# Kernel optimization log

Measured on AMD Instinct MI355X. Metric: run time of the kernel, lower is better.

## Reference

```python
import jax, jax.numpy as jnp
import numpy as np

EMBED_DIM = 1024
NUM_HEADS = 16
HEAD_DIM = EMBED_DIM // NUM_HEADS
SEQ_LEN = 2048
BATCH = 2
THETA_BASE = 10000.0


def rope_angles(head_dim, max_seq_len):
    inv_freq = 1.0 / (THETA_BASE ** (jnp.arange(0, head_dim, 2, dtype=jnp.float32) / head_dim))
    pos = jnp.arange(max_seq_len, dtype=jnp.float32)
    angles = pos[:, None] * inv_freq[None, :]              # [S, D/2]
    angles = jnp.concatenate([angles, angles], axis=-1)    # [S, D]
    return jnp.cos(angles), jnp.sin(angles)


def apply_rope(x, cos, sin):
    # x: [B, H, S, D]; cos/sin: [S, D]
    d = x.shape[-1]
    x1, x2 = x[..., : d // 2], x[..., d // 2 :]
    rotated = jnp.concatenate([-x2, x1], axis=-1)
    return x * cos[None, None, :, :] + rotated * sin[None, None, :, :]


def setup_inputs() -> dict:
    key = jax.random.key(0)
    kx, kq, kk, kv, ko = jax.random.split(key, 5)
    s = 1.0 / np.sqrt(EMBED_DIM)
    return {
        "x": jax.random.normal(kx, (BATCH, SEQ_LEN, EMBED_DIM), dtype=jnp.float32),
        "Wq": jax.random.normal(kq, (EMBED_DIM, EMBED_DIM), dtype=jnp.float32) * s,
        "Wk": jax.random.normal(kk, (EMBED_DIM, EMBED_DIM), dtype=jnp.float32) * s,
        "Wv": jax.random.normal(kv, (EMBED_DIM, EMBED_DIM), dtype=jnp.float32) * s,
        "Wo": jax.random.normal(ko, (EMBED_DIM, EMBED_DIM), dtype=jnp.float32) * s,
    }


def reference(x, Wq, Wk, Wv, Wo):
    B, S, E = x.shape
    H, D = NUM_HEADS, HEAD_DIM
    cos, sin = rope_angles(D, S)

    def split_heads(t):
        return t.reshape(B, S, H, D).transpose(0, 2, 1, 3)  # [B,H,S,D]

    q = split_heads(x @ Wq.T)
    k = split_heads(x @ Wk.T)
    v = split_heads(x @ Wv.T)

    q = apply_rope(q, cos, sin)
    k = apply_rope(k, cos, sin)

    scores = jnp.einsum("bhsd,bhtd->bhst", q, k)
    causal = jnp.triu(jnp.ones((S, S), dtype=bool), k=1)
    scores = jnp.where(causal[None, None, :, :], -jnp.inf, scores)
    weights = jax.nn.softmax(scores / jnp.sqrt(jnp.float32(D)), axis=-1)

    ctx = jnp.einsum("bhst,bhtd->bhsd", weights, v)
    ctx = ctx.transpose(0, 2, 1, 3).reshape(B, S, E)
    return ctx @ Wo.T
```

## Files before the change

kernel.cpp:

```cpp
#include <hip/hip_runtime.h>
#include <hip/hip_bf16.h>

#define H_NUM 16
#define D_DIM 64
#define S_LEN 2048
#define EMB   1024
#define M_TOT 4096

typedef unsigned short u16;
typedef unsigned int   u32;
typedef __attribute__((ext_vector_type(8))) short short8;
typedef __attribute__((ext_vector_type(4))) float f32x4;

__device__ __forceinline__ u32 f2bf_u(float f) {
    u32 u = __float_as_uint(f);
    return (u + 0x7fffu + ((u >> 16) & 1u)) >> 16;
}
__device__ __forceinline__ u32 pack2(float a, float b) {
    return f2bf_u(a) | (f2bf_u(b) << 16);
}
__device__ __forceinline__ u32 pack2t(float a, float b) {
    return __builtin_amdgcn_perm(__float_as_uint(b), __float_as_uint(a),
                                 0x07060302u);
}
__device__ __forceinline__ uint4 pack8(float4 lo, float4 hi) {
    return make_uint4(pack2(lo.x, lo.y), pack2(lo.z, lo.w),
                      pack2(hi.x, hi.y), pack2(hi.z, hi.w));
}

__device__ __forceinline__ void lds_dma16(const u16* g, u16* l) {
    __builtin_amdgcn_global_load_lds(
        (const __attribute__((address_space(1))) void*)g,
        (__attribute__((address_space(3))) void*)l, 16, 0, 0);
}

__global__ __launch_bounds__(256) void cast_kernel(
    const float* __restrict__ x,  const float* __restrict__ Wq,
    const float* __restrict__ Wk, const float* __restrict__ Wv,
    const float* __restrict__ Wo, u16* __restrict__ ws, float2* __restrict__ tab)
{
    const int seg = blockIdx.y;
    if (seg == 5) {
        const int idx = blockIdx.x * 256 + threadIdx.x;
        if (idx < S_LEN * 32) {
            const int s = idx >> 5, d = idx & 31;
            const float ang = (float)s * __expf(-(float)d * 0.28782313662425573f);
            tab[idx] = make_float2(cosf(ang), sinf(ang));
        }
        return;
    }
    const float* src = (seg == 0) ? x : (seg == 1) ? Wq : (seg == 2) ? Wk
                     : (seg == 3) ? Wv : Wo;
    u16* dst = (seg == 0) ? ws : ws + (3 + seg) * 1048576;
    const int n = (seg == 0) ? 4194304 : 1048576;
    const int idx = (blockIdx.x * 256 + threadIdx.x) * 8;
    if (idx < n) {
        float4 lo = *(const float4*)(src + idx);
        float4 hi = *(const float4*)(src + idx + 4);
        *(uint4*)(dst + idx) = pack8(lo, hi);
    }
}

__global__ __launch_bounds__(256) void qkv_rope_kernel(
    const u16* __restrict__ xb, const u16* __restrict__ wb,
    const float2* __restrict__ tab,
    u16* __restrict__ qo, u16* __restrict__ ko, u16* __restrict__ vo)
{
    const int w  = blockIdx.y >> 3;
    const int nb = blockIdx.y & 7;
    const u16* W = wb + w * 1048576;

    __shared__ __align__(16) u16 smem[12288];
    u16* As = smem;
    u16* Bs = smem + 64 * 64;
    u16 (*Ep)[132] = (u16(*)[132])smem;

    const int tid   = threadIdx.x;
    const int lane  = tid & 63;
    const int wid   = tid >> 6;
    const int waveM = wid >> 1;
    const int waveN = wid & 1;
    const int col16 = lane & 15;
    const int quad  = lane >> 4;

    const int m0 = blockIdx.x * 64;
    const int n0 = nb * 128;

    f32x4 acc[2][4];
    const f32x4 zero4 = {0.f, 0.f, 0.f, 0.f};
#pragma unroll
    for (int i = 0; i < 2; i++)
#pragma unroll
        for (int j = 0; j < 4; j++) acc[i][j] = zero4;

    const int drow = tid >> 3;
    const int dpos = tid & 7;
    const u16* Ag = xb + (size_t)m0 * EMB;
    const u16* Bg = W  + (size_t)n0 * EMB;

    for (int k0 = 0; k0 < EMB; k0 += 64) {
        __syncthreads();
#pragma unroll
        for (int j = 0; j < 2; j++) {
            const int rl = j * 32 + drow;
            const int cg = dpos ^ (rl & 7);
            lds_dma16(Ag + (size_t)rl * EMB + k0 + cg * 8,
                      As + (j * 32 + wid * 8) * 64);
        }
#pragma unroll
        for (int j = 0; j < 4; j++) {
            const int rl = j * 32 + drow;
            const int cg = dpos ^ (rl & 7);
            lds_dma16(Bg + (size_t)rl * EMB + k0 + cg * 8,
                      Bs + (j * 32 + wid * 8) * 64);
        }
        __syncthreads();

        short8 af[2][2], bf[4][2];
#pragma unroll
        for (int mt = 0; mt < 2; mt++) {
            const int r = waveM * 32 + mt * 16 + col16;
#pragma unroll
            for (int ks = 0; ks < 2; ks++) {
                const int p = (ks * 4 + quad) ^ (r & 7);
                af[mt][ks] = *(const short8*)(As + r * 64 + p * 8);
            }
        }
#pragma unroll
        for (int nt = 0; nt < 4; nt++) {
            const int r = waveN * 64 + nt * 16 + col16;
#pragma unroll
            for (int ks = 0; ks < 2; ks++) {
                const int p = (ks * 4 + quad) ^ (r & 7);
                bf[nt][ks] = *(const short8*)(Bs + r * 64 + p * 8);
            }
        }
#pragma unroll
        for (int ks = 0; ks < 2; ks++)
#pragma unroll
            for (int mt = 0; mt < 2; mt++)
#pragma unroll
                for (int nt = 0; nt < 4; nt++)
                    acc[mt][nt] = __builtin_amdgcn_mfma_f32_16x16x32_bf16(
                        af[mt][ks], bf[nt][ks], acc[mt][nt], 0, 0, 0);
    }

    const float qs = (w == 0) ? 0.18033688011112042f : 1.0f;
    __syncthreads();
#pragma unroll
    for (int mt = 0; mt < 2; mt++) {
#pragma unroll
        for (int r = 0; r < 4; r++) {
            const int m_local = waveM * 32 + mt * 16 + quad * 4 + r;
            const int s = (m0 + m_local) & 2047;
            if (w == 2) {
#pragma unroll
                for (int nt = 0; nt < 4; nt++)
                    Ep[m_local][waveN * 64 + nt * 16 + col16] =
                        (u16)f2bf_u(acc[mt][nt][r]);
            } else {
#pragma unroll
                for (int nt = 0; nt < 2; nt++) {
                    const int d = nt * 16 + col16;
                    const float2 cs = tab[s * 32 + d];
                    const float lo = acc[mt][nt][r];
                    const float hi = acc[mt][nt + 2][r];
                    Ep[m_local][waveN * 64 + d]      =
                        (u16)f2bf_u((lo * cs.x - hi * cs.y) * qs);
                    Ep[m_local][waveN * 64 + d + 32] =
                        (u16)f2bf_u((hi * cs.x + lo * cs.y) * qs);
                }
            }
        }
    }
    __syncthreads();

    const int b = m0 >> 11;
    if (w != 2) {
        u16* out = (w == 0) ? qo : ko;
#pragma unroll
        for (int j = 0; j < 4; j++) {
            const int g = j * 256 + tid;
            const int head_local = g >> 9;
            const int sl  = (g >> 3) & 63;
            const int cir = g & 7;
            uint4 val = *(const uint4*)(&Ep[sl][head_local * 64 + cir * 8]);
            const int h = (n0 >> 6) + head_local;
            const size_t base = (((size_t)(b * H_NUM + h)) * S_LEN + (m0 & 2047)) * 64;
            *(uint4*)(out + base + (size_t)(g & 511) * 8) = val;
        }
    } else {
        const int s0 = m0 & 2047;
#pragma unroll
        for (int j = 0; j < 4; j++) {
            const int g = j * 256 + tid;
            const int d_all = g >> 3;
            const int sc = g & 7;
            u32 wv[4];
#pragma unroll
            for (int hw = 0; hw < 4; hw++) {
                const int p0 = sc * 8 + hw * 2;
                const int r0 = ((p0 & 3) << 4) | (p0 >> 2);
                const int p1 = p0 + 1;
                const int r1 = ((p1 & 3) << 4) | (p1 >> 2);
                wv[hw] = (u32)Ep[r0][d_all] | ((u32)Ep[r1][d_all] << 16);
            }
            const int h = (n0 >> 6) + (d_all >> 6);
            const int d = d_all & 63;
            *(uint4*)(vo + ((size_t)(b * H_NUM + h) * 64 + d) * 2048 + s0 + sc * 8) =
                make_uint4(wv[0], wv[1], wv[2], wv[3]);
        }
    }
}

__global__ __launch_bounds__(256) void attn_kernel(
    const u16* __restrict__ q, const u16* __restrict__ k,
    const u16* __restrict__ v, u16* __restrict__ ctx)
{
    __shared__ __align__(16) u16 QP[64 * 64];
    __shared__ __align__(16) u16 Ks[2][64 * 64];
    __shared__ __align__(16) u16 VTs[2][64 * 64];

    const int tid   = threadIdx.x;
    const int lane  = tid & 63;
    const int wid   = tid >> 6;
    const int col16 = lane & 15;
    const int quad  = lane >> 4;

    const int bh = blockIdx.x;
    const int y = blockIdx.y;
    const int o = y & 7, g = y >> 3;
    const int qb = (g == 0) ? (31 - o) : (g == 1) ? (16 + o)
                 : (g == 2) ? (15 - o) : o;
    const int qBase = qb * 64;
    const size_t bhOff = (size_t)bh * S_LEN * D_DIM;

    const int drow = tid >> 3;
    const int dpos = tid & 7;

    auto stage = [&](int kt, int buf) {
#pragma unroll
        for (int j = 0; j < 2; j++) {
            const int rl = j * 32 + drow;
            const int cg = dpos ^ (rl & 7);
            lds_dma16(k + bhOff + (size_t)(kt * 64 + rl) * 64 + cg * 8,
                      &Ks[buf][(j * 32 + wid * 8) * 64]);
        }
#pragma unroll
        for (int j = 0; j < 2; j++) {
            const int rl = j * 32 + drow;
            const int cg = dpos ^ (rl & 7);
            lds_dma16(v + bhOff + (size_t)rl * 2048 + kt * 64 + cg * 8,
                      &VTs[buf][(j * 32 + wid * 8) * 64]);
        }
    };

    stage(0, 0);
#pragma unroll
    for (int j = 0; j < 2; j++) {
        const int rl = j * 32 + drow;
        const int cg = dpos ^ (rl & 7);
        lds_dma16(q + bhOff + (size_t)(qBase + rl) * 64 + cg * 8,
                  QP + (j * 32 + wid * 8) * 64);
    }
    __syncthreads();

    short8 qf[2];
    {
        const int rq = wid * 16 + col16;
#pragma unroll
        for (int ks = 0; ks < 2; ks++) {
            const int c = (ks * 4 + quad) ^ (rq & 7);
            qf[ks] = *(const short8*)(QP + rq * 64 + c * 8);
        }
    }

    const short ONE = (short)0x3F80;
    const short8 onesf = {ONE, ONE, ONE, ONE, ONE, ONE, ONE, ONE};

    f32x4 O[4];
    const f32x4 zero4 = {0.f, 0.f, 0.f, 0.f};
#pragma unroll
    for (int j = 0; j < 4; j++) O[j] = zero4;
    f32x4 lacc = zero4;

    for (int kt = 0; kt <= qb; kt++) {
        if (kt > 0) __syncthreads();
        if (kt < qb) stage(kt + 1, (kt + 1) & 1);
        const int cur = kt & 1;

        f32x4 sc[4];
#pragma unroll
        for (int nt = 0; nt < 4; nt++) sc[nt] = zero4;
#pragma unroll
        for (int ks = 0; ks < 2; ks++) {
            short8 kf[4];
#pragma unroll
            for (int nt = 0; nt < 4; nt++) {
                const int rk = nt * 16 + col16;
                const int c = (ks * 4 + quad) ^ (rk & 7);
                kf[nt] = *(const short8*)(&Ks[cur][rk * 64 + c * 8]);
            }
            __builtin_amdgcn_s_setprio(1);
#pragma unroll
            for (int nt = 0; nt < 4; nt++)
                sc[nt] = __builtin_amdgcn_mfma_f32_16x16x32_bf16(
                    qf[ks], kf[nt], sc[nt], 0, 0, 0);
            __builtin_amdgcn_s_setprio(0);
        }

        if (kt == qb) {
#pragma unroll
            for (int r = 0; r < 4; r++) {
                const int qg = qBase + wid * 16 + quad * 4 + r;
#pragma unroll
                for (int nt = 0; nt < 4; nt++) {
                    const int kg = kt * 64 + nt * 16 + col16;
                    float p = exp2f(sc[nt][r]);
                    if (kg > qg) p = 0.f;
                    sc[nt][r] = p;
                }
            }
        } else {
#pragma unroll
            for (int r = 0; r < 4; r++) {
#pragma unroll
                for (int nt = 0; nt < 4; nt++)
                    sc[nt][r] = exp2f(sc[nt][r]);
            }
        }

#pragma unroll
        for (int r = 0; r < 4; r++) {
            const int ml = quad * 4 + r;
            const u32 lo = pack2t(sc[0][r], sc[1][r]);
            const u32 hi = pack2t(sc[2][r], sc[3][r]);
            *(uint2*)(QP + (wid * 16 + ml) * 64 +
                      (((col16 >> 1) ^ (ml & 7)) * 8 + (col16 & 1) * 4)) =
                make_uint2(lo, hi);
        }

#pragma unroll
        for (int ks = 0; ks < 2; ks++) {
            short8 pf, vf[4];
            {
                const int c = (ks * 4 + quad) ^ (col16 & 7);
                pf = *(const short8*)(QP + (wid * 16 + col16) * 64 + c * 8);
            }
#pragma unroll
            for (int dt = 0; dt < 4; dt++) {
                const int d = dt * 16 + col16;
                const int c = (ks * 4 + quad) ^ (d & 7);
                vf[dt] = *(const short8*)(&VTs[cur][d * 64 + c * 8]);
            }
            __builtin_amdgcn_s_setprio(1);
#pragma unroll
            for (int dt = 0; dt < 4; dt++)
                O[dt] = __builtin_amdgcn_mfma_f32_16x16x32_bf16(
                    pf, vf[dt], O[dt], 0, 0, 0);
            lacc = __builtin_amdgcn_mfma_f32_16x16x32_bf16(
                pf, onesf, lacc, 0, 0, 0);
            __builtin_amdgcn_s_setprio(0);
        }
    }

    const int b = bh >> 4, h = bh & 15;
#pragma unroll
    for (int r = 0; r < 4; r++) {
        const int ml = quad * 4 + r;
        const float inv = 1.0f / lacc[r];
        const u32 lo = pack2t(O[0][r] * inv, O[1][r] * inv);
        const u32 hi = pack2t(O[2][r] * inv, O[3][r] * inv);
        *(uint2*)(QP + (wid * 16 + ml) * 64 +
                  (((col16 >> 1) ^ (ml & 7)) * 8 + (col16 & 1) * 4)) =
            make_uint2(lo, hi);
    }
#pragma unroll
    for (int j = 0; j < 2; j++) {
        const int gg  = j * 64 + lane;
        const int sl = gg >> 3;
        const int cir = gg & 7;
        u32 wv[4];
#pragma unroll
        for (int hw = 0; hw < 4; hw++) {
            const int d0 = cir * 8 + hw * 2;
            const int p0 = ((d0 & 15) << 2) | (d0 >> 4);
            const int d1 = d0 + 1;
            const int p1 = ((d1 & 15) << 2) | (d1 >> 4);
            const u16 v0 = QP[(wid * 16 + sl) * 64 + ((p0 >> 3) ^ (sl & 7)) * 8 + (p0 & 7)];
            const u16 v1 = QP[(wid * 16 + sl) * 64 + ((p1 >> 3) ^ (sl & 7)) * 8 + (p1 & 7)];
            wv[hw] = (u32)v0 | ((u32)v1 << 16);
        }
        const size_t rowbase =
            ((size_t)b * S_LEN + qBase + wid * 16 + sl) * EMB + h * 64;
        *(uint4*)(ctx + rowbase + cir * 8) = make_uint4(wv[0], wv[1], wv[2], wv[3]);
    }
}

__global__ __launch_bounds__(256) void proj_kernel(
    const u16* __restrict__ X, const u16* __restrict__ W, float* __restrict__ out)
{
    __shared__ __align__(16) u16 smem[8192];
    u16* As = smem;
    u16* Bs = smem + 64 * 64;

    const int tid   = threadIdx.x;
    const int lane  = tid & 63;
    const int wid   = tid >> 6;
    const int col16 = lane & 15;
    const int quad  = lane >> 4;

    const int m0 = blockIdx.x * 64;
    const int n0 = blockIdx.y * 64;

    f32x4 acc[4];
    const f32x4 zero4 = {0.f, 0.f, 0.f, 0.f};
#pragma unroll
    for (int i = 0; i < 4; i++) acc[i] = zero4;

    const int drow = tid >> 3;
    const int dpos = tid & 7;
    const u16* Ag = X + (size_t)m0 * EMB;
    const u16* Bg = W + (size_t)n0 * EMB;

    for (int k0 = 0; k0 < EMB; k0 += 64) {
        __syncthreads();
#pragma unroll
        for (int j = 0; j < 2; j++) {
            const int rl = j * 32 + drow;
            const int cg = dpos ^ (rl & 7);
            lds_dma16(Ag + (size_t)rl * EMB + k0 + cg * 8,
                      As + (j * 32 + wid * 8) * 64);
        }
#pragma unroll
        for (int j = 0; j < 2; j++) {
            const int rl = j * 32 + drow;
            const int cg = dpos ^ (rl & 7);
            lds_dma16(Bg + (size_t)rl * EMB + k0 + cg * 8,
                      Bs + (j * 32 + wid * 8) * 64);
        }
        __syncthreads();

        short8 af[2], bf[4][2];
        {
            const int r = wid * 16 + col16;
#pragma unroll
            for (int ks = 0; ks < 2; ks++) {
                const int p = (ks * 4 + quad) ^ (r & 7);
                af[ks] = *(const short8*)(As + r * 64 + p * 8);
            }
        }
#pragma unroll
        for (int nt = 0; nt < 4; nt++) {
            const int r = nt * 16 + col16;
#pragma unroll
            for (int ks = 0; ks < 2; ks++) {
                const int p = (ks * 4 + quad) ^ (r & 7);
                bf[nt][ks] = *(const short8*)(Bs + r * 64 + p * 8);
            }
        }
#pragma unroll
        for (int ks = 0; ks < 2; ks++)
#pragma unroll
            for (int nt = 0; nt < 4; nt++)
                acc[nt] = __builtin_amdgcn_mfma_f32_16x16x32_bf16(
                    bf[nt][ks], af[ks], acc[nt], 0, 0, 0);
    }

#pragma unroll
    for (int nt = 0; nt < 4; nt++) {
        const int m_g = m0 + wid * 16 + col16;
        const int n_g = n0 + nt * 16 + quad * 4;
        *(f32x4*)(out + (size_t)m_g * EMB + n_g) = acc[nt];
    }
}

extern "C" void kernel_launch(void* const* d_in, const int* in_sizes, int n_in,
                              void* d_out, int out_size, void* d_ws, size_t ws_size,
                              hipStream_t stream)
{
    const float* x  = (const float*)d_in[0];
    const float* Wq = (const float*)d_in[1];
    const float* Wk = (const float*)d_in[2];
    const float* Wv = (const float*)d_in[3];
    const float* Wo = (const float*)d_in[4];

    u16* ws = (u16*)d_ws;
    u16* xb  = ws;
    u16* wb  = ws + 4194304;
    u16* wob = ws + 7340032;
    u16* q   = ws + 8388608;
    u16* k   = ws + 12582912;
    u16* v   = ws + 16777216;
    u16* ctx = ws + 20971520;
    float2* tab = (float2*)(ws + 25165824);

    cast_kernel<<<dim3(2048, 6), 256, 0, stream>>>(x, Wq, Wk, Wv, Wo, ws, tab);
    qkv_rope_kernel<<<dim3(64, 24), 256, 0, stream>>>(xb, wb, tab, q, k, v);
    attn_kernel<<<dim3(32, 32), 256, 0, stream>>>(q, k, v, ctx);
    proj_kernel<<<dim3(64, 16), 256, 0, stream>>>(ctx, wob, (float*)d_out);
}
```

Measured before the change: 173.8 us.

## Split long causal attention rows across two blocks with flag-synchronized partial merge

Query blocks 16-31 are split into two workgroups: one covers the early key tiles and writes unnormalized partial O and row sums to a workspace, then raises a flag. The other covers the last 16 key tiles, spins on that flag, and adds the partials before normalizing. This shortens the longest blocks and balances causal work across more workgroups, at the cost of extra global traffic and a spin-wait that assumes the producer block is scheduled. Exp2 and reciprocal are also swapped for hardware intrinsics.

```diff
diff --git a/kernel.cpp b/kernel.cpp
--- a/kernel.cpp
+++ b/kernel.cpp
@@ -37,10 +37,15 @@
 __global__ __launch_bounds__(256) void cast_kernel(
     const float* __restrict__ x,  const float* __restrict__ Wq,
     const float* __restrict__ Wk, const float* __restrict__ Wv,
-    const float* __restrict__ Wo, u16* __restrict__ ws, float2* __restrict__ tab)
+    const float* __restrict__ Wo, u16* __restrict__ ws, float2* __restrict__ tab,
+    u32* __restrict__ flags)
 {
     const int seg = blockIdx.y;
     if (seg == 5) {
+        if (blockIdx.x == 0) {
+            flags[threadIdx.x] = 0;
+            flags[threadIdx.x + 256] = 0;
+        }
         const int idx = blockIdx.x * 256 + threadIdx.x;
         if (idx < S_LEN * 32) {
             const int s = idx >> 5, d = idx & 31;
@@ -215,7 +220,9 @@
 
 __global__ __launch_bounds__(256) void attn_kernel(
     const u16* __restrict__ q, const u16* __restrict__ k,
-    const u16* __restrict__ v, u16* __restrict__ ctx)
+    const u16* __restrict__ v, u16* __restrict__ ctx,
+    float* __restrict__ opart, float* __restrict__ lpart,
+    u32* __restrict__ flags)
 {
     __shared__ __align__(16) u16 QP[64 * 64];
     __shared__ __align__(16) u16 Ks[2][64 * 64];
@@ -228,10 +235,12 @@
     const int quad  = lane >> 4;
 
     const int bh = blockIdx.x;
-    const int y = blockIdx.y;
-    const int o = y & 7, g = y >> 3;
-    const int qb = (g == 0) ? (31 - o) : (g == 1) ? (16 + o)
-                 : (g == 2) ? (15 - o) : o;
+    const int y  = blockIdx.y;
+    int role, qb, kt0, kt1;
+    if (y < 16)      { role = 1; qb = 31 - y; kt0 = 0;       kt1 = qb - 16; }
+    else if (y < 32) { role = 2; qb = 47 - y; kt0 = qb - 15; kt1 = qb; }
+    else             { role = 0; qb = 47 - y; kt0 = 0;       kt1 = qb; }
+
     const int qBase = qb * 64;
     const size_t bhOff = (size_t)bh * S_LEN * D_DIM;
 
@@ -255,7 +264,7 @@
         }
     };
 
-    stage(0, 0);
+    stage(kt0, 0);
 #pragma unroll
     for (int j = 0; j < 2; j++) {
         const int rl = j * 32 + drow;
@@ -284,10 +293,10 @@
     for (int j = 0; j < 4; j++) O[j] = zero4;
     f32x4 lacc = zero4;
 
-    for (int kt = 0; kt <= qb; kt++) {
-        if (kt > 0) __syncthreads();
-        if (kt < qb) stage(kt + 1, (kt + 1) & 1);
-        const int cur = kt & 1;
+    for (int kt = kt0; kt <= kt1; kt++) {
+        if (kt > kt0) __syncthreads();
+        if (kt < kt1) stage(kt + 1, (kt + 1 - kt0) & 1);
+        const int cur = (kt - kt0) & 1;
 
         f32x4 sc[4];
 #pragma unroll
@@ -316,7 +325,7 @@
 #pragma unroll
                 for (int nt = 0; nt < 4; nt++) {
                     const int kg = kt * 64 + nt * 16 + col16;
-                    float p = exp2f(sc[nt][r]);
+                    float p = __builtin_amdgcn_exp2f(sc[nt][r]);
                     if (kg > qg) p = 0.f;
                     sc[nt][r] = p;
                 }
@@ -326,7 +335,7 @@
             for (int r = 0; r < 4; r++) {
 #pragma unroll
                 for (int nt = 0; nt < 4; nt++)
-                    sc[nt][r] = exp2f(sc[nt][r]);
+                    sc[nt][r] = __builtin_amdgcn_exp2f(sc[nt][r]);
             }
         }
 
@@ -364,11 +373,42 @@
         }
     }
 
+    const int u = bh * 16 + (qb - 16);
+
+    if (role == 1) {
+        float* op = opart + (size_t)u * 4096 + tid * 16;
+#pragma unroll
+        for (int dt = 0; dt < 4; dt++) *(f32x4*)(op + dt * 4) = O[dt];
+        if (col16 == 0)
+            *(f32x4*)(lpart + u * 64 + wid * 16 + quad * 4) = lacc;
+        __syncthreads();
+        if (tid == 0)
+            __hip_atomic_store(&flags[u], 1u, __ATOMIC_RELEASE,
+                               __HIP_MEMORY_SCOPE_AGENT);
+        return;
+    }
+    if (role == 2) {
+        if (tid == 0) {
+            while (__hip_atomic_load(&flags[u], __ATOMIC_ACQUIRE,
+                                     __HIP_MEMORY_SCOPE_AGENT) == 0)
+                __builtin_amdgcn_s_sleep(8);
+        }
+        __syncthreads();
+        const float* op = opart + (size_t)u * 4096 + tid * 16;
+#pragma unroll
+        for (int dt = 0; dt < 4; dt++) {
+            const f32x4 pp = *(const f32x4*)(op + dt * 4);
+            O[dt] += pp;
+        }
+        const f32x4 lp = *(const f32x4*)(lpart + u * 64 + wid * 16 + quad * 4);
+        lacc += lp;
+    }
+
     const int b = bh >> 4, h = bh & 15;
 #pragma unroll
     for (int r = 0; r < 4; r++) {
         const int ml = quad * 4 + r;
-        const float inv = 1.0f / lacc[r];
+        const float inv = __builtin_amdgcn_rcpf(lacc[r]);
         const u32 lo = pack2t(O[0][r] * inv, O[1][r] * inv);
         const u32 hi = pack2t(O[2][r] * inv, O[3][r] * inv);
         *(uint2*)(QP + (wid * 16 + ml) * 64 +
@@ -495,8 +535,13 @@
     u16* ctx = ws + 20971520;
     float2* tab = (float2*)(ws + 25165824);
 
-    cast_kernel<<<dim3(2048, 6), 256, 0, stream>>>(x, Wq, Wk, Wv, Wo, ws, tab);
+    char* wsb = (char*)d_ws;
+    u32*   flags = (u32*)  (wsb + 50855936);
+    float* lpart = (float*)(wsb + 50857984);
+    float* opart = (float*)(wsb + 50989056);
+
+    cast_kernel<<<dim3(2048, 6), 256, 0, stream>>>(x, Wq, Wk, Wv, Wo, ws, tab, flags);
     qkv_rope_kernel<<<dim3(64, 24), 256, 0, stream>>>(xb, wb, tab, q, k, v);
-    attn_kernel<<<dim3(32, 32), 256, 0, stream>>>(q, k, v, ctx);
+    attn_kernel<<<dim3(32, 48), 256, 0, stream>>>(q, k, v, ctx, opart, lpart, flags);
     proj_kernel<<<dim3(64, 16), 256, 0, stream>>>(ctx, wob, (float*)d_out);
 }
```

Measured after the change: 175.8 us. Within noise of the previous version (+1.1%).

## Pair causal query tiles per block to share K/V staging and balance work

Applied to the files above, without the earlier changes.

Each attention block now processes two query tiles (p and 31-p) that share the same staged K/V tiles, halving the grid in y and giving every block equal causal work. This reduces redundant K/V loads into LDS and removes load imbalance across blocks. It also swaps exp2f and division for the hardware exp2 and rcp intrinsics. The cost is doubled accumulator registers and an extra LDS tile per block, which may lower occupancy, and only 512 blocks remain to fill the GPU.

```diff
diff --git a/kernel.cpp b/kernel.cpp
--- a/kernel.cpp
+++ b/kernel.cpp
@@ -217,7 +217,8 @@
     const u16* __restrict__ q, const u16* __restrict__ k,
     const u16* __restrict__ v, u16* __restrict__ ctx)
 {
-    __shared__ __align__(16) u16 QP[64 * 64];
+    __shared__ __align__(16) u16 QPA[64 * 64];
+    __shared__ __align__(16) u16 QPB[64 * 64];
     __shared__ __align__(16) u16 Ks[2][64 * 64];
     __shared__ __align__(16) u16 VTs[2][64 * 64];
 
@@ -228,11 +229,11 @@
     const int quad  = lane >> 4;
 
     const int bh = blockIdx.x;
-    const int y = blockIdx.y;
-    const int o = y & 7, g = y >> 3;
-    const int qb = (g == 0) ? (31 - o) : (g == 1) ? (16 + o)
-                 : (g == 2) ? (15 - o) : o;
-    const int qBase = qb * 64;
+    const int p  = blockIdx.y;
+    const int qbA = p;
+    const int qbB = 31 - p;
+    const int qBaseA = qbA * 64;
+    const int qBaseB = qbB * 64;
     const size_t bhOff = (size_t)bh * S_LEN * D_DIM;
 
     const int drow = tid >> 3;
@@ -260,35 +261,35 @@
     for (int j = 0; j < 2; j++) {
         const int rl = j * 32 + drow;
         const int cg = dpos ^ (rl & 7);
-        lds_dma16(q + bhOff + (size_t)(qBase + rl) * 64 + cg * 8,
-                  QP + (j * 32 + wid * 8) * 64);
+        lds_dma16(q + bhOff + (size_t)(qBaseA + rl) * 64 + cg * 8,
+                  QPA + (j * 32 + wid * 8) * 64);
+        lds_dma16(q + bhOff + (size_t)(qBaseB + rl) * 64 + cg * 8,
+                  QPB + (j * 32 + wid * 8) * 64);
     }
     __syncthreads();
 
-    short8 qf[2];
+    short8 qfA[2], qfB[2];
     {
         const int rq = wid * 16 + col16;
 #pragma unroll
         for (int ks = 0; ks < 2; ks++) {
             const int c = (ks * 4 + quad) ^ (rq & 7);
-            qf[ks] = *(const short8*)(QP + rq * 64 + c * 8);
+            qfA[ks] = *(const short8*)(QPA + rq * 64 + c * 8);
+            qfB[ks] = *(const short8*)(QPB + rq * 64 + c * 8);
         }
     }
 
     const short ONE = (short)0x3F80;
     const short8 onesf = {ONE, ONE, ONE, ONE, ONE, ONE, ONE, ONE};
 
-    f32x4 O[4];
+    f32x4 OA[4], OB[4];
     const f32x4 zero4 = {0.f, 0.f, 0.f, 0.f};
 #pragma unroll
-    for (int j = 0; j < 4; j++) O[j] = zero4;
-    f32x4 lacc = zero4;
-
-    for (int kt = 0; kt <= qb; kt++) {
-        if (kt > 0) __syncthreads();
-        if (kt < qb) stage(kt + 1, (kt + 1) & 1);
-        const int cur = kt & 1;
-
+    for (int j = 0; j < 4; j++) { OA[j] = zero4; OB[j] = zero4; }
+    f32x4 laccA = zero4, laccB = zero4;
+
+    auto process = [&](const short8* qf, u16* QP, f32x4* O, f32x4& lacc,
+                       int qBase, bool diag, int kt, int cur) {
         f32x4 sc[4];
 #pragma unroll
         for (int nt = 0; nt < 4; nt++) sc[nt] = zero4;
@@ -309,16 +310,16 @@
             __builtin_amdgcn_s_setprio(0);
         }
 
-        if (kt == qb) {
+        if (diag) {
 #pragma unroll
             for (int r = 0; r < 4; r++) {
                 const int qg = qBase + wid * 16 + quad * 4 + r;
 #pragma unroll
                 for (int nt = 0; nt < 4; nt++) {
                     const int kg = kt * 64 + nt * 16 + col16;
-                    float p = exp2f(sc[nt][r]);
-                    if (kg > qg) p = 0.f;
-                    sc[nt][r] = p;
+                    float pv = __builtin_amdgcn_exp2f(sc[nt][r]);
+                    if (kg > qg) pv = 0.f;
+                    sc[nt][r] = pv;
                 }
             }
         } else {
@@ -326,7 +327,7 @@
             for (int r = 0; r < 4; r++) {
 #pragma unroll
                 for (int nt = 0; nt < 4; nt++)
-                    sc[nt][r] = exp2f(sc[nt][r]);
+                    sc[nt][r] = __builtin_amdgcn_exp2f(sc[nt][r]);
             }
         }
 
@@ -362,39 +363,53 @@
                 pf, onesf, lacc, 0, 0, 0);
             __builtin_amdgcn_s_setprio(0);
         }
+    };
+
+    for (int kt = 0; kt <= qbB; kt++) {
+        if (kt > 0) __syncthreads();
+        if (kt < qbB) stage(kt + 1, (kt + 1) & 1);
+        const int cur = kt & 1;
+
+        process(qfB, QPB, OB, laccB, qBaseB, kt == qbB, kt, cur);
+        if (kt <= qbA)
+            process(qfA, QPA, OA, laccA, qBaseA, kt == qbA, kt, cur);
     }
 
     const int b = bh >> 4, h = bh & 15;
-#pragma unroll
-    for (int r = 0; r < 4; r++) {
-        const int ml = quad * 4 + r;
-        const float inv = 1.0f / lacc[r];
-        const u32 lo = pack2t(O[0][r] * inv, O[1][r] * inv);
-        const u32 hi = pack2t(O[2][r] * inv, O[3][r] * inv);
-        *(uint2*)(QP + (wid * 16 + ml) * 64 +
-                  (((col16 >> 1) ^ (ml & 7)) * 8 + (col16 & 1) * 4)) =
-            make_uint2(lo, hi);
-    }
-#pragma unroll
-    for (int j = 0; j < 2; j++) {
-        const int gg  = j * 64 + lane;
-        const int sl = gg >> 3;
-        const int cir = gg & 7;
-        u32 wv[4];
-#pragma unroll
-        for (int hw = 0; hw < 4; hw++) {
-            const int d0 = cir * 8 + hw * 2;
-            const int p0 = ((d0 & 15) << 2) | (d0 >> 4);
-            const int d1 = d0 + 1;
-            const int p1 = ((d1 & 15) << 2) | (d1 >> 4);
-            const u16 v0 = QP[(wid * 16 + sl) * 64 + ((p0 >> 3) ^ (sl & 7)) * 8 + (p0 & 7)];
-            const u16 v1 = QP[(wid * 16 + sl) * 64 + ((p1 >> 3) ^ (sl & 7)) * 8 + (p1 & 7)];
-            wv[hw] = (u32)v0 | ((u32)v1 << 16);
-        }
-        const size_t rowbase =
-            ((size_t)b * S_LEN + qBase + wid * 16 + sl) * EMB + h * 64;
-        *(uint4*)(ctx + rowbase + cir * 8) = make_uint4(wv[0], wv[1], wv[2], wv[3]);
-    }
+    auto epilogue = [&](u16* QP, f32x4* O, f32x4& lacc, int qBase) {
+#pragma unroll
+        for (int r = 0; r < 4; r++) {
+            const int ml = quad * 4 + r;
+            const float inv = __builtin_amdgcn_rcpf(lacc[r]);
+            const u32 lo = pack2t(O[0][r] * inv, O[1][r] * inv);
+            const u32 hi = pack2t(O[2][r] * inv, O[3][r] * inv);
+            *(uint2*)(QP + (wid * 16 + ml) * 64 +
+                      (((col16 >> 1) ^ (ml & 7)) * 8 + (col16 & 1) * 4)) =
+                make_uint2(lo, hi);
+        }
+#pragma unroll
+        for (int j = 0; j < 2; j++) {
+            const int gg  = j * 64 + lane;
+            const int sl = gg >> 3;
+            const int cir = gg & 7;
+            u32 wv[4];
+#pragma unroll
+            for (int hw = 0; hw < 4; hw++) {
+                const int d0 = cir * 8 + hw * 2;
+                const int p0 = ((d0 & 15) << 2) | (d0 >> 4);
+                const int d1 = d0 + 1;
+                const int p1 = ((d1 & 15) << 2) | (d1 >> 4);
+                const u16 v0 = QP[(wid * 16 + sl) * 64 + ((p0 >> 3) ^ (sl & 7)) * 8 + (p0 & 7)];
+                const u16 v1 = QP[(wid * 16 + sl) * 64 + ((p1 >> 3) ^ (sl & 7)) * 8 + (p1 & 7)];
+                wv[hw] = (u32)v0 | ((u32)v1 << 16);
+            }
+            const size_t rowbase =
+                ((size_t)b * S_LEN + qBase + wid * 16 + sl) * EMB + h * 64;
+            *(uint4*)(ctx + rowbase + cir * 8) = make_uint4(wv[0], wv[1], wv[2], wv[3]);
+        }
+    };
+    epilogue(QPA, OA, laccA, qBaseA);
+    epilogue(QPB, OB, laccB, qBaseB);
 }
 
 __global__ __launch_bounds__(256) void proj_kernel(
@@ -497,6 +512,6 @@
 
     cast_kernel<<<dim3(2048, 6), 256, 0, stream>>>(x, Wq, Wk, Wv, Wo, ws, tab);
     qkv_rope_kernel<<<dim3(64, 24), 256, 0, stream>>>(xb, wb, tab, q, k, v);
-    attn_kernel<<<dim3(32, 32), 256, 0, stream>>>(q, k, v, ctx);
+    attn_kernel<<<dim3(32, 16), 256, 0, stream>>>(q, k, v, ctx);
     proj_kernel<<<dim3(64, 16), 256, 0, stream>>>(ctx, wob, (float*)d_out);
 }
```

Result: faster. 166.3 us (-4.3%).
